# Performance work log

Hardware: AMD Instinct MI355X
Metric: run time of the kernel (lower is better)

The kernel has to match this reference:

```python
import jax, jax.numpy as jnp
import numpy as np

N0 = 16384; F_IN = 384; H = 512; E0 = 131072
DEPTH = 2; RATIO = 0.25; START_K = 6; K_INC = 1; INTERP_K = 6


def _pdist2(a, b):
    # squared euclidean distances [Na, Nb]
    d2 = jnp.sum(a * a, axis=1)[:, None] + jnp.sum(b * b, axis=1)[None, :] - 2.0 * (a @ b.T)
    return jnp.maximum(d2, 0.0)


def _fps(pos, n_keep):
    # farthest point sampling, deterministic start at node 0
    sel0 = jnp.zeros((n_keep,), jnp.int32)
    dist0 = jnp.sum((pos - pos[0]) ** 2, axis=-1)

    def body(i, st):
        sel, dist = st
        idx = jnp.argmax(dist).astype(jnp.int32)
        sel = sel.at[i].set(idx)
        dist = jnp.minimum(dist, jnp.sum((pos - pos[idx]) ** 2, axis=-1))
        return (sel, dist)

    sel, _ = jax.lax.fori_loop(1, n_keep, body, (sel0, dist0))
    return sel


def _knn_graph(pos, k):
    n = pos.shape[0]
    d2 = _pdist2(pos, pos)
    d2 = d2.at[jnp.arange(n), jnp.arange(n)].set(1e10)  # exclude self
    _, nbr = jax.lax.top_k(-d2, k)                      # [n, k] nearest neighbors
    src = nbr.reshape(-1)                               # flow: source_to_target
    dst = jnp.repeat(jnp.arange(n, dtype=nbr.dtype), k)
    return src, dst


def _gcn(x, src, dst, W, b):
    # GCNConv(improved=True): A_hat = D^-1/2 (A + 2I) D^-1/2, edge weights = 1
    n = x.shape[0]
    h = x @ W
    deg = jax.ops.segment_sum(jnp.ones(src.shape[0], x.dtype), dst, num_segments=n) + 2.0
    dinv = jax.lax.rsqrt(deg)
    coef = dinv[src] * dinv[dst]
    agg = jax.ops.segment_sum(h[src] * coef[:, None], dst, num_segments=n)
    agg = agg + h * (2.0 * dinv * dinv)[:, None]        # self loops with weight 2
    return agg + b


def _knn_interpolate(x, pos_x, pos_y, k):
    # interpolate coarse features x at pos_x onto fine positions pos_y (PyG knn_interpolate)
    d2 = _pdist2(pos_y, pos_x)                          # [Ny, Nx]
    negd, idx = jax.lax.top_k(-d2, k)                   # k nearest coarse points
    w = 1.0 / jnp.maximum(-negd, 1e-16)                 # [Ny, k]
    num = jnp.einsum('yk,ykf->yf', w, x[idx])
    return num / jnp.sum(w, axis=-1, keepdims=True)


def setup_inputs() -> dict:
    key = jax.random.key(0)
    ks = jax.random.split(key, 16)
    def w(k, fin, fout):
        return (jax.random.normal(k, (fin, fout), jnp.float32) / np.sqrt(fin)).astype(jnp.float32)
    return {
        'x': jax.random.normal(ks[0], (N0, F_IN), jnp.float32),
        'pos': jax.random.uniform(ks[1], (N0, 2), jnp.float32) * 100.0,
        'edge_index': jax.random.randint(ks[2], (2, E0), 0, N0, dtype=jnp.int32),
        'W_down0': w(ks[3], F_IN, H), 'b_down0': jnp.zeros((H,), jnp.float32),
        'W_down1': w(ks[4], H, H),   'b_down1': jnp.zeros((H,), jnp.float32),
        'W_up0': w(ks[5], H, H),     'b_up0': jnp.zeros((H,), jnp.float32),
        'W_up1': w(ks[6], H, H),     'b_up1': jnp.zeros((H,), jnp.float32),
        'W_lin': w(ks[7], H, H),     'b_lin': jnp.zeros((H,), jnp.float32),
    }


def reference(x, pos, edge_index, W_down0, b_down0, W_down1, b_down1,
              W_up0, b_up0, W_up1, b_up1, W_lin, b_lin):
    src, dst = edge_index[0], edge_index[1]
    Wd = [(W_down0, b_down0), (W_down1, b_down1)]
    Wu = [(W_up0, b_up0), (W_up1, b_up1)]
    all_pos = [pos]
    all_edges = [(src, dst)]
    for i in range(DEPTH):
        x = jax.nn.relu(_gcn(x, src, dst, *Wd[i]))
        n_keep = int(x.shape[0] * RATIO)
        perm = _fps(jax.lax.stop_gradient(pos), n_keep)
        pos = pos[perm]
        src, dst = _knn_graph(pos, START_K + i * K_INC)
        x = x[perm]
        all_pos.append(pos)
        all_edges.append((src, dst))
    for i in range(DEPTH):
        x = _knn_interpolate(x, all_pos[-i - 1], all_pos[-i - 2], INTERP_K)
        s, d = all_edges[-i - 2]
        x = jax.nn.relu(_gcn(x, s, d, *Wu[i]))
    return x @ W_lin + b_lin
```

## Files before the change

### kernel.cpp

```cpp
#include <hip/hip_runtime.h>

#define N0 16384
#define N1 4096
#define N2 1024
#define E0C 131072
#define FIN 384
#define HF 512

__device__ inline float4 f4fma(float w, const float4 v, float4 a) {
  a.x = fmaf(w, v.x, a.x); a.y = fmaf(w, v.y, a.y);
  a.z = fmaf(w, v.z, a.z); a.w = fmaf(w, v.w, a.w);
  return a;
}

__global__ __launch_bounds__(256)
void count_deg(const int* __restrict__ dst, int* __restrict__ cnt, int E) {
  int e = blockIdx.x * 256 + threadIdx.x;
  if (e < E) atomicAdd(&cnt[dst[e]], 1);
}

__global__ __launch_bounds__(1024)
void scan_offsets(const int* __restrict__ cnt, int* __restrict__ offs,
                  float* __restrict__ dinv) {
  __shared__ int ts[1024];
  const int t = threadIdx.x;
  int local[16];
  int sum = 0;
  #pragma unroll
  for (int j = 0; j < 16; ++j) { local[j] = cnt[t * 16 + j]; sum += local[j]; }
  ts[t] = sum;
  __syncthreads();
  for (int off = 1; off < 1024; off <<= 1) {
    int v = (t >= off) ? ts[t - off] : 0;
    __syncthreads();
    ts[t] += v;
    __syncthreads();
  }
  int run = ts[t] - sum;
  #pragma unroll
  for (int j = 0; j < 16; ++j) {
    offs[t * 16 + j] = run;
    dinv[t * 16 + j] = 1.0f / sqrtf((float)local[j] + 2.0f);
    run += local[j];
  }
  if (t == 1023) offs[N0] = run;
}

__global__ __launch_bounds__(256)
void fill_csr(const int* __restrict__ src, const int* __restrict__ dst,
              const int* __restrict__ offs, int* __restrict__ cursor,
              int* __restrict__ srcl, int E) {
  int e = blockIdx.x * 256 + threadIdx.x;
  if (e < E) {
    int d = dst[e];
    int p = atomicAdd(&cursor[d], 1);
    srcl[offs[d] + p] = src[e];
  }
}

template<int BM, int BN, int BK>
__global__ __launch_bounds__(256)
void gemm_f32(const float* __restrict__ A, const float* __restrict__ W,
              const float* __restrict__ bias, float* __restrict__ C,
              int M, int N, int K, int addBias) {
  __shared__ float As[BK][BM + 4];
  __shared__ float Ws[BK][BN];
  const int tid = threadIdx.x;
  const int bm = blockIdx.x * BM;
  const int bn = blockIdx.y * BN;
  const int tx = tid & 15;
  const int ty = tid >> 4;
  float acc[8][4];
  #pragma unroll
  for (int i = 0; i < 8; ++i)
    #pragma unroll
    for (int j = 0; j < 4; ++j) acc[i][j] = 0.f;

  for (int k0 = 0; k0 < K; k0 += BK) {
    #pragma unroll
    for (int h = 0; h < (BM * BK) / (256 * 4); ++h) {
      int q = tid + h * 256;
      int r = q >> 2;
      int c = (q & 3) << 2;
      float4 v = *(const float4*)(A + (size_t)(bm + r) * K + k0 + c);
      As[c][r] = v.x; As[c + 1][r] = v.y; As[c + 2][r] = v.z; As[c + 3][r] = v.w;
    }
    {
      int kk = tid >> 4;
      int n = (tid & 15) << 2;
      *(float4*)(&Ws[kk][n]) = *(const float4*)(W + (size_t)(k0 + kk) * N + bn + n);
    }
    __syncthreads();
    #pragma unroll
    for (int kk = 0; kk < BK; ++kk) {
      float4 b4 = *(const float4*)(&Ws[kk][tx << 2]);
      float4 a0 = *(const float4*)(&As[kk][ty << 3]);
      float4 a1 = *(const float4*)(&As[kk][(ty << 3) + 4]);
      float a[8] = {a0.x, a0.y, a0.z, a0.w, a1.x, a1.y, a1.z, a1.w};
      float b[4] = {b4.x, b4.y, b4.z, b4.w};
      #pragma unroll
      for (int i = 0; i < 8; ++i)
        #pragma unroll
        for (int j = 0; j < 4; ++j)
          acc[i][j] = fmaf(a[i], b[j], acc[i][j]);
    }
    __syncthreads();
  }
  #pragma unroll
  for (int i = 0; i < 8; ++i) {
    int row = bm + (ty << 3) + i;
    float4 o = {acc[i][0], acc[i][1], acc[i][2], acc[i][3]};
    if (addBias) {
      const float4 bb = *(const float4*)(bias + bn + (tx << 2));
      o.x += bb.x; o.y += bb.y; o.z += bb.z; o.w += bb.w;
    }
    *(float4*)(C + (size_t)row * N + bn + (tx << 2)) = o;
  }
}

__global__ __launch_bounds__(256)
void gcn_agg_csr(const float* __restrict__ h, const int* __restrict__ offs,
                 const int* __restrict__ srcl, const float* __restrict__ dinv,
                 const float* __restrict__ bias, float* __restrict__ out, int n) {
  const int wid = threadIdx.x >> 6, lane = threadIdx.x & 63;
  const int node = blockIdx.x * 4 + wid;
  if (node >= n) return;
  const float di = dinv[node];
  const int s0 = offs[node], s1 = offs[node + 1];
  float4 a0 = {0, 0, 0, 0}, a1 = {0, 0, 0, 0};
  for (int e = s0; e < s1; ++e) {
    const int s = srcl[e];
    const float w = dinv[s] * di;
    const float4* r = (const float4*)(h + (size_t)s * HF);
    a0 = f4fma(w, r[lane], a0);
    a1 = f4fma(w, r[64 + lane], a1);
  }
  const float sw = 2.0f * di * di;
  const float4* rs = (const float4*)(h + (size_t)node * HF);
  a0 = f4fma(sw, rs[lane], a0);
  a1 = f4fma(sw, rs[64 + lane], a1);
  const float4 b0 = *(const float4*)(bias + (lane << 2));
  const float4 b1 = *(const float4*)(bias + 256 + (lane << 2));
  a0.x = fmaxf(a0.x + b0.x, 0.f); a0.y = fmaxf(a0.y + b0.y, 0.f);
  a0.z = fmaxf(a0.z + b0.z, 0.f); a0.w = fmaxf(a0.w + b0.w, 0.f);
  a1.x = fmaxf(a1.x + b1.x, 0.f); a1.y = fmaxf(a1.y + b1.y, 0.f);
  a1.z = fmaxf(a1.z + b1.z, 0.f); a1.w = fmaxf(a1.w + b1.w, 0.f);
  float4* o = (float4*)(out + (size_t)node * HF);
  o[lane] = a0; o[64 + lane] = a1;
}

template<int K>
__global__ __launch_bounds__(256)
void gcn_agg_knn(const float* __restrict__ h, const int* __restrict__ nbr,
                 const float* __restrict__ bias, float* __restrict__ out, int n) {
  const int wid = threadIdx.x >> 6, lane = threadIdx.x & 63;
  const int node = blockIdx.x * 4 + wid;
  if (node >= n) return;
  const float di = 1.0f / sqrtf((float)(K + 2));
  const float w = di * di;
  float4 a0 = {0, 0, 0, 0}, a1 = {0, 0, 0, 0};
  #pragma unroll
  for (int j = 0; j < K; ++j) {
    const int s = nbr[node * K + j];
    const float4* r = (const float4*)(h + (size_t)s * HF);
    a0 = f4fma(w, r[lane], a0);
    a1 = f4fma(w, r[64 + lane], a1);
  }
  const float sw = 2.0f * di * di;
  const float4* rs = (const float4*)(h + (size_t)node * HF);
  a0 = f4fma(sw, rs[lane], a0);
  a1 = f4fma(sw, rs[64 + lane], a1);
  const float4 b0 = *(const float4*)(bias + (lane << 2));
  const float4 b1 = *(const float4*)(bias + 256 + (lane << 2));
  a0.x = fmaxf(a0.x + b0.x, 0.f); a0.y = fmaxf(a0.y + b0.y, 0.f);
  a0.z = fmaxf(a0.z + b0.z, 0.f); a0.w = fmaxf(a0.w + b0.w, 0.f);
  a1.x = fmaxf(a1.x + b1.x, 0.f); a1.y = fmaxf(a1.y + b1.y, 0.f);
  a1.z = fmaxf(a1.z + b1.z, 0.f); a1.w = fmaxf(a1.w + b1.w, 0.f);
  float4* o = (float4*)(out + (size_t)node * HF);
  o[lane] = a0; o[64 + lane] = a1;
}

__device__ __forceinline__ unsigned part1by1(unsigned x) {
  x &= 0xFFFFu;
  x = (x | (x << 8)) & 0x00FF00FFu;
  x = (x | (x << 4)) & 0x0F0F0F0Fu;
  x = (x | (x << 2)) & 0x33333333u;
  x = (x | (x << 1)) & 0x55555555u;
  return x;
}

__global__ __launch_bounds__(256)
void bin_hist(const float* __restrict__ pos, int* __restrict__ cid,
              int* __restrict__ hist, int n) {
  int i = blockIdx.x * 256 + threadIdx.x;
  if (i >= n) return;
  float x = pos[2 * i], y = pos[2 * i + 1];
  int cxi = (int)(x * 0.32f); cxi = cxi < 0 ? 0 : (cxi > 31 ? 31 : cxi);
  int cyi = (int)(y * 0.32f); cyi = cyi < 0 ? 0 : (cyi > 31 ? 31 : cyi);
  int c = (int)(part1by1((unsigned)cxi) | (part1by1((unsigned)cyi) << 1));
  cid[i] = c;
  atomicAdd(&hist[c], 1);
}

__global__ __launch_bounds__(1024)
void bin_scan(const int* __restrict__ hist, int* __restrict__ offs) {
  __shared__ int ts[1024];
  const int t = threadIdx.x;
  int v = hist[t];
  ts[t] = v;
  __syncthreads();
  for (int off = 1; off < 1024; off <<= 1) {
    int u = (t >= off) ? ts[t - off] : 0;
    __syncthreads();
    ts[t] += u;
    __syncthreads();
  }
  offs[t] = ts[t] - v;
  if (t == 1023) offs[1024] = ts[t];
}

__global__ __launch_bounds__(256)
void bin_scatter(const float* __restrict__ pos, const int* __restrict__ cid,
                 const int* __restrict__ offs, int* __restrict__ cursor,
                 float* __restrict__ sx, float* __restrict__ sy,
                 int* __restrict__ sid, int n) {
  int i = blockIdx.x * 256 + threadIdx.x;
  if (i >= n) return;
  int c = cid[i];
  int p = atomicAdd(&cursor[c], 1);
  int slot = offs[c] + p;
  sx[slot] = pos[2 * i];
  sy[slot] = pos[2 * i + 1];
  sid[slot] = i;
}

template<int NN>
__device__ __forceinline__ unsigned ror16(unsigned v) {
  return (unsigned)__builtin_amdgcn_update_dpp(0, (int)v, 0x120 | NN, 0xF, 0xF, false);
}

__device__ __forceinline__ void kcmp(unsigned& hi, unsigned& lo, float& x, float& y,
                                     unsigned ohi, unsigned olo, float ox, float oy) {
  unsigned long long a = ((unsigned long long)hi << 32) | lo;
  unsigned long long b = ((unsigned long long)ohi << 32) | olo;
  if (b > a) { hi = ohi; lo = olo; x = ox; y = oy; }
}

#define ROR_STEP(NN) { \
    unsigned ohi_ = ror16<NN>(hi), olo_ = ror16<NN>(lo); \
    unsigned ox_ = ror16<NN>(__float_as_uint(x)), oy_ = ror16<NN>(__float_as_uint(y)); \
    kcmp(hi, lo, x, y, ohi_, olo_, __uint_as_float(ox_), __uint_as_float(oy_)); }

__device__ __forceinline__ void wave_entry_reduce(
    unsigned long long ckey, float ccx, float ccy, int t, float4* wsc,
    unsigned& ehi, unsigned& elo, float& ex, float& ey) {
  unsigned hi = (unsigned)(ckey >> 32), lo = (unsigned)ckey;
  float x = ccx, y = ccy;
  ROR_STEP(1) ROR_STEP(2) ROR_STEP(4) ROR_STEP(8)
  if ((t & 15) == 0)
    wsc[(t >> 4) & 3] = make_float4(__uint_as_float(hi), __uint_as_float(lo), x, y);
  float4 a0 = wsc[0], a1 = wsc[1], a2 = wsc[2], a3 = wsc[3];
  hi = __float_as_uint(a0.x); lo = __float_as_uint(a0.y); x = a0.z; y = a0.w;
  kcmp(hi, lo, x, y, __float_as_uint(a1.x), __float_as_uint(a1.y), a1.z, a1.w);
  kcmp(hi, lo, x, y, __float_as_uint(a2.x), __float_as_uint(a2.y), a2.z, a2.w);
  kcmp(hi, lo, x, y, __float_as_uint(a3.x), __float_as_uint(a3.y), a3.z, a3.w);
  ehi = hi; elo = lo; ex = x; ey = y;
}

template<int N, int NT, int CPB, int SUBMAX, int NKEEP>
__global__ __launch_bounds__(NT, 1)
void fps_fast7(const float* __restrict__ pos0,
               const float* __restrict__ sx, const float* __restrict__ sy,
               const int* __restrict__ sid, const int* __restrict__ coffs,
               int* __restrict__ perm, float* __restrict__ pos_out) {
  constexpr int NW = NT / 64;
  const int t = threadIdx.x, wid = t >> 6, lane = t & 63;

  __shared__ float2 pp[N];
  __shared__ float4 ebuf[2][NW];
  __shared__ float4 wscr[NW][4];

  unsigned long long key[SUBMAX];

  const int start = coffs[wid * CPB];
  const int end   = coffs[wid * CPB + CPB];
  const int base  = start + lane;

  float cx = pos0[0], cy = pos0[1];
  if (t == 0) { perm[0] = 0; pos_out[0] = cx; pos_out[1] = cy; }

  float x0 = 3.4e38f, x1 = -3.4e38f, y0 = 3.4e38f, y1 = -3.4e38f;
  unsigned long long ckey = 0; float ccx = 0.f, ccy = 0.f;
  #pragma unroll
  for (int j = 0; j < SUBMAX; ++j) {
    int idx = base + j * 64;
    bool v = idx < end;
    int ridx = idx < (N - 1) ? idx : (N - 1);
    float qx = sx[ridx], qy = sy[ridx];
    unsigned uid = ~(unsigned)sid[ridx];
    if (v) {
      pp[idx] = make_float2(qx, qy);
      x0 = fminf(x0, qx); x1 = fmaxf(x1, qx);
      y0 = fminf(y0, qy); y1 = fmaxf(y1, qy);
    }
    float dx = __fsub_rn(qx, cx), dy = __fsub_rn(qy, cy);
    float nd = __fadd_rn(__fmul_rn(dx, dx), __fmul_rn(dy, dy));
    unsigned long long k =
        v ? (((unsigned long long)__float_as_uint(nd) << 32) | uid) : 0ull;
    key[j] = k;
    if (k > ckey) { ckey = k; ccx = qx; ccy = qy; }
  }

  #pragma unroll
  for (int m = 1; m < 64; m <<= 1) {
    x0 = fminf(x0, __shfl_xor(x0, m)); x1 = fmaxf(x1, __shfl_xor(x1, m));
    y0 = fminf(y0, __shfl_xor(y0, m)); y1 = fmaxf(y1, __shfl_xor(y1, m));
  }

  unsigned ehi, elo; float ex, ey;
  wave_entry_reduce(ckey, ccx, ccy, t, wscr[wid], ehi, elo, ex, ey);
  if (lane == 0)
    ebuf[0][wid] = make_float4(__uint_as_float(ehi), __uint_as_float(elo), ex, ey);
  __syncthreads();

  int p = 0;
  for (int i = 1; i < NKEEP; ++i) {
    float4 e = ebuf[p][t & (NW - 1)];
    unsigned hi = __float_as_uint(e.x), lo = __float_as_uint(e.y);
    float x = e.z, y = e.w;
    ROR_STEP(1)
    if constexpr (NW >= 4)  { ROR_STEP(2) }
    if constexpr (NW >= 8)  { ROR_STEP(4) }
    if constexpr (NW >= 16) { ROR_STEP(8) }
    if (t == 0) {
      perm[i] = (int)(~lo);
      pos_out[2 * i] = x; pos_out[2 * i + 1] = y;
    }
    cx = x; cy = y;

    float mdx = fmaxf(fmaxf(__fsub_rn(x0, cx), __fsub_rn(cx, x1)), 0.f);
    float mdy = fmaxf(fmaxf(__fsub_rn(y0, cy), __fsub_rn(cy, y1)), 0.f);
    float mb = mdx * mdx + mdy * mdy;
    if (!(mb * 0.99999f > __uint_as_float(ehi))) {
      unsigned long long bk = 0; float bx = 0.f, by = 0.f;
      #pragma unroll
      for (int j = 0; j < SUBMAX; ++j) {
        int idx = base + j * 64;
        int ridx = idx < (N - 1) ? idx : (N - 1);
        float2 q = pp[ridx];
        float dx = __fsub_rn(q.x, cx), dy = __fsub_rn(q.y, cy);
        float nd = __fadd_rn(__fmul_rn(dx, dx), __fmul_rn(dy, dy));
        unsigned long long nk =
            ((unsigned long long)__float_as_uint(nd) << 32) | (unsigned)key[j];
        if (nk < key[j]) key[j] = nk;
        if (key[j] > bk) { bk = key[j]; bx = q.x; by = q.y; }
      }
      wave_entry_reduce(bk, bx, by, t, wscr[wid], ehi, elo, ex, ey);
    }
    if (lane == 0)
      ebuf[p ^ 1][wid] = make_float4(__uint_as_float(ehi), __uint_as_float(elo), ex, ey);
    __syncthreads();
    p ^= 1;
  }
}

__global__ __launch_bounds__(256)
void gather_rows(const float* __restrict__ xin, const int* __restrict__ perm,
                 float* __restrict__ xout, int n) {
  const int wid = threadIdx.x >> 6, lane = threadIdx.x & 63;
  const int i = blockIdx.x * 4 + wid;
  if (i >= n) return;
  const int s = perm[i];
  const float4* r = (const float4*)(xin + (size_t)s * HF);
  float4* o = (float4*)(xout + (size_t)i * HF);
  o[lane] = r[lane];
  o[64 + lane] = r[64 + lane];
}

template<int NPTS, int K>
__global__ __launch_bounds__(256)
void knn_graph_kernel(const float* __restrict__ pos, int* __restrict__ srcout) {
  __shared__ float sx[NPTS], sy[NPTS], ss[NPTS];
  const int tid = threadIdx.x;
  for (int idx = tid; idx < NPTS; idx += 256) {
    float x = pos[2 * idx], y = pos[2 * idx + 1];
    sx[idx] = x; sy[idx] = y;
    ss[idx] = __fadd_rn(__fmul_rn(x, x), __fmul_rn(y, y));
  }
  __syncthreads();
  const int q = blockIdx.x * 256 + tid;
  const float qx = sx[q], qy = sy[q], qs = ss[q];
  float bd[K]; int bi[K];
  #pragma unroll
  for (int m = 0; m < K; ++m) { bd[m] = 3.4e38f; bi[m] = 0; }
  for (int j = 0; j < NPTS; ++j) {
    if (j == q) continue;
    float dot = __fadd_rn(__fmul_rn(qx, sx[j]), __fmul_rn(qy, sy[j]));
    float d2 = fmaxf(__fsub_rn(__fadd_rn(qs, ss[j]), __fmul_rn(2.0f, dot)), 0.0f);
    if (d2 < bd[K - 1]) {
      bool pr[K];
      #pragma unroll
      for (int m = 0; m < K; ++m) pr[m] = (d2 < bd[m]);
      #pragma unroll
      for (int m = K - 1; m >= 1; --m) {
        bd[m] = pr[m] ? (pr[m - 1] ? bd[m - 1] : d2) : bd[m];
        bi[m] = pr[m] ? (pr[m - 1] ? bi[m - 1] : j) : bi[m];
      }
      if (pr[0]) { bd[0] = d2; bi[0] = j; }
    }
  }
  #pragma unroll
  for (int m = 0; m < K; ++m) srcout[q * K + m] = bi[m];
}

template<int NX, int K>
__global__ __launch_bounds__(256)
void interp_topk(const float* __restrict__ posy, const float* __restrict__ posx,
                 int* __restrict__ oidx, float* __restrict__ ow,
                 float* __restrict__ owsum) {
  __shared__ float sx[NX], sy[NX], ss[NX];
  const int tid = threadIdx.x;
  for (int idx = tid; idx < NX; idx += 256) {
    float x = posx[2 * idx], y = posx[2 * idx + 1];
    sx[idx] = x; sy[idx] = y;
    ss[idx] = __fadd_rn(__fmul_rn(x, x), __fmul_rn(y, y));
  }
  __syncthreads();
  const int q = blockIdx.x * 256 + tid;
  const float qx = posy[2 * q], qy = posy[2 * q + 1];
  const float qs = __fadd_rn(__fmul_rn(qx, qx), __fmul_rn(qy, qy));
  float bd[K]; int bi[K];
  #pragma unroll
  for (int m = 0; m < K; ++m) { bd[m] = 3.4e38f; bi[m] = 0; }
  for (int j = 0; j < NX; ++j) {
    float dot = __fadd_rn(__fmul_rn(qx, sx[j]), __fmul_rn(qy, sy[j]));
    float d2 = fmaxf(__fsub_rn(__fadd_rn(qs, ss[j]), __fmul_rn(2.0f, dot)), 0.0f);
    if (d2 < bd[K - 1]) {
      bool pr[K];
      #pragma unroll
      for (int m = 0; m < K; ++m) pr[m] = (d2 < bd[m]);
      #pragma unroll
      for (int m = K - 1; m >= 1; --m) {
        bd[m] = pr[m] ? (pr[m - 1] ? bd[m - 1] : d2) : bd[m];
        bi[m] = pr[m] ? (pr[m - 1] ? bi[m - 1] : j) : bi[m];
      }
      if (pr[0]) { bd[0] = d2; bi[0] = j; }
    }
  }
  float wsum = 0.f;
  #pragma unroll
  for (int m = 0; m < K; ++m) {
    float w = 1.0f / fmaxf(bd[m], 1e-16f);
    ow[q * K + m] = w;
    oidx[q * K + m] = bi[m];
    wsum = __fadd_rn(wsum, w);
  }
  owsum[q] = wsum;
}

template<int K>
__global__ __launch_bounds__(256)
void interp_combine(const float* __restrict__ xin, const int* __restrict__ idx,
                    const float* __restrict__ w, const float* __restrict__ wsum,
                    float* __restrict__ out, int ny) {
  const int wid = threadIdx.x >> 6, lane = threadIdx.x & 63;
  const int q = blockIdx.x * 4 + wid;
  if (q >= ny) return;
  float4 a0 = {0, 0, 0, 0}, a1 = {0, 0, 0, 0};
  #pragma unroll
  for (int m = 0; m < K; ++m) {
    const int s = idx[q * K + m];
    const float wk = w[q * K + m];
    const float4* r = (const float4*)(xin + (size_t)s * HF);
    a0 = f4fma(wk, r[lane], a0);
    a1 = f4fma(wk, r[64 + lane], a1);
  }
  const float inv = wsum[q];
  a0.x /= inv; a0.y /= inv; a0.z /= inv; a0.w /= inv;
  a1.x /= inv; a1.y /= inv; a1.z /= inv; a1.w /= inv;
  float4* o = (float4*)(out + (size_t)q * HF);
  o[lane] = a0; o[64 + lane] = a1;
}

extern "C" void kernel_launch(void* const* d_in, const int* in_sizes, int n_in,
                              void* d_out, int out_size, void* d_ws, size_t ws_size,
                              hipStream_t stream) {
  const float* x    = (const float*)d_in[0];
  const float* pos  = (const float*)d_in[1];
  const int*   ei   = (const int*)d_in[2];
  const float* Wd0  = (const float*)d_in[3];
  const float* bd0  = (const float*)d_in[4];
  const float* Wd1  = (const float*)d_in[5];
  const float* bd1  = (const float*)d_in[6];
  const float* Wu0  = (const float*)d_in[7];
  const float* bu0  = (const float*)d_in[8];
  const float* Wu1  = (const float*)d_in[9];
  const float* bu1  = (const float*)d_in[10];
  const float* Wl   = (const float*)d_in[11];
  const float* bl   = (const float*)d_in[12];
  float* out = (float*)d_out;

  char* ws = (char*)d_ws;
  size_t off = 0;
  auto alloc = [&](size_t bytes) -> char* {
    char* p = ws + off;
    off = (off + bytes + 255) & ~(size_t)255;
    return p;
  };
  float* bufA   = (float*)alloc((size_t)N0 * HF * 4);
  float* bufB   = (float*)alloc((size_t)N0 * HF * 4);
  float* bufC   = (float*)alloc((size_t)N1 * HF * 4);
  float* x2     = (float*)alloc((size_t)N2 * HF * 4);
  int*   offs0  = (int*)alloc((N0 + 1) * 4);
  int*   srcl0  = (int*)alloc(E0C * 4);
  int*   cnt    = (int*)alloc(N0 * 4);
  int*   cursor = (int*)alloc(N0 * 4);
  float* dinv0  = (float*)alloc(N0 * 4);
  int*   perm0  = (int*)alloc(N1 * 4);
  float* pos1   = (float*)alloc(N1 * 2 * 4);
  int*   src1   = (int*)alloc(N1 * 6 * 4);
  int*   perm1  = (int*)alloc(N2 * 4);
  float* pos2   = (float*)alloc(N2 * 2 * 4);
  int*   iidx   = (int*)alloc((size_t)N0 * 6 * 4);
  float* iw     = (float*)alloc((size_t)N0 * 6 * 4);
  float* iwsum  = (float*)alloc(N0 * 4);
  float* bsx    = (float*)alloc(N0 * 4);
  float* bsy    = (float*)alloc(N0 * 4);
  int*   bsid   = (int*)alloc(N0 * 4);
  int*   bcid   = (int*)alloc(N0 * 4);
  int*   bhist  = (int*)alloc(1024 * 4);
  int*   bcur   = (int*)alloc(1024 * 4);
  int*   boffs  = (int*)alloc(1025 * 4);

  float* h1   = bufB;
  float* x1f  = bufB + (size_t)N1 * HF;
  float* hu0  = bufB;
  float* xu0f = bufB + (size_t)N1 * HF;

  hipMemsetAsync(cnt, 0, N0 * 4, stream);
  hipMemsetAsync(cursor, 0, N0 * 4, stream);
  count_deg<<<E0C / 256, 256, 0, stream>>>(ei + E0C, cnt, E0C);
  scan_offsets<<<1, 1024, 0, stream>>>(cnt, offs0, dinv0);
  fill_csr<<<E0C / 256, 256, 0, stream>>>(ei, ei + E0C, offs0, cursor, srcl0, E0C);

  hipMemsetAsync(bhist, 0, 1024 * 4, stream);
  hipMemsetAsync(bcur, 0, 1024 * 4, stream);
  bin_hist<<<N0 / 256, 256, 0, stream>>>(pos, bcid, bhist, N0);
  bin_scan<<<1, 1024, 0, stream>>>(bhist, boffs);
  bin_scatter<<<N0 / 256, 256, 0, stream>>>(pos, bcid, boffs, bcur, bsx, bsy, bsid, N0);

  gemm_f32<128, 64, 16><<<dim3(N0 / 128, HF / 64), 256, 0, stream>>>(
      x, Wd0, nullptr, bufA, N0, HF, FIN, 0);
  gcn_agg_csr<<<N0 / 4, 256, 0, stream>>>(bufA, offs0, srcl0, dinv0, bd0, bufB, N0);
  fps_fast7<N0, 1024, 64, 19, N1><<<1, 1024, 0, stream>>>(pos, bsx, bsy, bsid, boffs, perm0, pos1);
  gather_rows<<<N1 / 4, 256, 0, stream>>>(bufB, perm0, bufC, N1);
  knn_graph_kernel<N1, 6><<<N1 / 256, 256, 0, stream>>>(pos1, src1);

  hipMemsetAsync(bhist, 0, 1024 * 4, stream);
  hipMemsetAsync(bcur, 0, 1024 * 4, stream);
  bin_hist<<<N1 / 256, 256, 0, stream>>>(pos1, bcid, bhist, N1);
  bin_scan<<<1, 1024, 0, stream>>>(bhist, boffs);
  bin_scatter<<<N1 / 256, 256, 0, stream>>>(pos1, bcid, boffs, bcur, bsx, bsy, bsid, N1);

  gemm_f32<128, 64, 16><<<dim3(N1 / 128, HF / 64), 256, 0, stream>>>(
      bufC, Wd1, nullptr, h1, N1, HF, HF, 0);
  gcn_agg_knn<6><<<N1 / 4, 256, 0, stream>>>(h1, src1, bd1, x1f, N1);
  fps_fast7<N1, 512, 128, 10, N2><<<1, 512, 0, stream>>>(pos1, bsx, bsy, bsid, boffs, perm1, pos2);
  gather_rows<<<N2 / 4, 256, 0, stream>>>(x1f, perm1, x2, N2);

  interp_topk<N2, 6><<<N1 / 256, 256, 0, stream>>>(pos1, pos2, iidx, iw, iwsum);
  interp_combine<6><<<N1 / 4, 256, 0, stream>>>(x2, iidx, iw, iwsum, bufC, N1);
  gemm_f32<128, 64, 16><<<dim3(N1 / 128, HF / 64), 256, 0, stream>>>(
      bufC, Wu0, nullptr, hu0, N1, HF, HF, 0);
  gcn_agg_knn<6><<<N1 / 4, 256, 0, stream>>>(hu0, src1, bu0, xu0f, N1);

  interp_topk<N1, 6><<<N0 / 256, 256, 0, stream>>>(pos, pos1, iidx, iw, iwsum);
  interp_combine<6><<<N0 / 4, 256, 0, stream>>>(xu0f, iidx, iw, iwsum, bufA, N0);
  gemm_f32<128, 64, 16><<<dim3(N0 / 128, HF / 64), 256, 0, stream>>>(
      bufA, Wu1, nullptr, bufB, N0, HF, HF, 0);
  gcn_agg_csr<<<N0 / 4, 256, 0, stream>>>(bufB, offs0, srcl0, dinv0, bu1, bufA, N0);

  gemm_f32<128, 64, 16><<<dim3(N0 / 128, HF / 64), 256, 0, stream>>>(
      bufA, Wl, bl, out, N0, HF, HF, 1);
}
```

Baseline: 7.859 ms.

## Give each FPS wave several spatial sub-blocks with per-block bounding-box skipping

The farthest point sampling kernel now assigns multiple spatial cell groups (NSUB) to each wave. Each sub-block keeps its own bounding box and cached best key, so a wave skips the distance update per sub-block rather than for its whole region. Fewer waves (512 and 256 threads instead of 1024 and 512) shorten the per-iteration cross-wave reduction and barrier. The cost is more registers per thread and more serial work per wave when sub-blocks are not skipped.

```diff
diff --git a/kernel.cpp b/kernel.cpp
--- a/kernel.cpp
+++ b/kernel.cpp
@@ -267,9 +267,9 @@
   ehi = hi; elo = lo; ex = x; ey = y;
 }
 
-template<int N, int NT, int CPB, int SUBMAX, int NKEEP>
+template<int N, int NT, int NSUB, int CPB, int SUBMAX, int NKEEP>
 __global__ __launch_bounds__(NT, 1)
-void fps_fast7(const float* __restrict__ pos0,
+void fps_fast8(const float* __restrict__ pos0,
                const float* __restrict__ sx, const float* __restrict__ sy,
                const int* __restrict__ sid, const int* __restrict__ coffs,
                int* __restrict__ perm, float* __restrict__ pos_out) {
@@ -280,45 +280,54 @@
   __shared__ float4 ebuf[2][NW];
   __shared__ float4 wscr[NW][4];
 
-  unsigned long long key[SUBMAX];
-
-  const int start = coffs[wid * CPB];
-  const int end   = coffs[wid * CPB + CPB];
-  const int base  = start + lane;
+  unsigned long long key[NSUB * SUBMAX];
+  int   bstart[NSUB], bend[NSUB];
+  float bx0[NSUB], bx1[NSUB], by0[NSUB], by1[NSUB];
+  unsigned bthi[NSUB], btlo[NSUB]; float btx[NSUB], bty[NSUB];
 
   float cx = pos0[0], cy = pos0[1];
   if (t == 0) { perm[0] = 0; pos_out[0] = cx; pos_out[1] = cy; }
 
-  float x0 = 3.4e38f, x1 = -3.4e38f, y0 = 3.4e38f, y1 = -3.4e38f;
-  unsigned long long ckey = 0; float ccx = 0.f, ccy = 0.f;
-  #pragma unroll
-  for (int j = 0; j < SUBMAX; ++j) {
-    int idx = base + j * 64;
-    bool v = idx < end;
-    int ridx = idx < (N - 1) ? idx : (N - 1);
-    float qx = sx[ridx], qy = sy[ridx];
-    unsigned uid = ~(unsigned)sid[ridx];
-    if (v) {
-      pp[idx] = make_float2(qx, qy);
-      x0 = fminf(x0, qx); x1 = fmaxf(x1, qx);
-      y0 = fminf(y0, qy); y1 = fmaxf(y1, qy);
-    }
-    float dx = __fsub_rn(qx, cx), dy = __fsub_rn(qy, cy);
-    float nd = __fadd_rn(__fmul_rn(dx, dx), __fmul_rn(dy, dy));
-    unsigned long long k =
-        v ? (((unsigned long long)__float_as_uint(nd) << 32) | uid) : 0ull;
-    key[j] = k;
-    if (k > ckey) { ckey = k; ccx = qx; ccy = qy; }
-  }
-
-  #pragma unroll
-  for (int m = 1; m < 64; m <<= 1) {
-    x0 = fminf(x0, __shfl_xor(x0, m)); x1 = fmaxf(x1, __shfl_xor(x1, m));
-    y0 = fminf(y0, __shfl_xor(y0, m)); y1 = fmaxf(y1, __shfl_xor(y1, m));
-  }
-
-  unsigned ehi, elo; float ex, ey;
-  wave_entry_reduce(ckey, ccx, ccy, t, wscr[wid], ehi, elo, ex, ey);
+  #pragma unroll
+  for (int s = 0; s < NSUB; ++s) {
+    const int b = wid * NSUB + s;
+    const int start = coffs[b * CPB];
+    const int end   = coffs[b * CPB + CPB];
+    bstart[s] = start; bend[s] = end;
+    float x0 = 3.4e38f, x1 = -3.4e38f, y0 = 3.4e38f, y1 = -3.4e38f;
+    unsigned long long bk = 0; float bkx = 0.f, bky = 0.f;
+    #pragma unroll
+    for (int j = 0; j < SUBMAX; ++j) {
+      int idx = start + lane + j * 64;
+      bool v = idx < end;
+      int ridx = idx < (N - 1) ? idx : (N - 1);
+      float qx = sx[ridx], qy = sy[ridx];
+      unsigned uid = ~(unsigned)sid[ridx];
+      if (v) {
+        pp[idx] = make_float2(qx, qy);
+        x0 = fminf(x0, qx); x1 = fmaxf(x1, qx);
+        y0 = fminf(y0, qy); y1 = fmaxf(y1, qy);
+      }
+      float dx = __fsub_rn(qx, cx), dy = __fsub_rn(qy, cy);
+      float nd = __fadd_rn(__fmul_rn(dx, dx), __fmul_rn(dy, dy));
+      unsigned long long k =
+          v ? (((unsigned long long)__float_as_uint(nd) << 32) | uid) : 0ull;
+      key[s * SUBMAX + j] = k;
+      if (k > bk) { bk = k; bkx = qx; bky = qy; }
+    }
+    #pragma unroll
+    for (int m = 1; m < 64; m <<= 1) {
+      x0 = fminf(x0, __shfl_xor(x0, m)); x1 = fmaxf(x1, __shfl_xor(x1, m));
+      y0 = fminf(y0, __shfl_xor(y0, m)); y1 = fmaxf(y1, __shfl_xor(y1, m));
+    }
+    bx0[s] = x0; bx1[s] = x1; by0[s] = y0; by1[s] = y1;
+    wave_entry_reduce(bk, bkx, bky, t, wscr[wid], bthi[s], btlo[s], btx[s], bty[s]);
+  }
+
+  unsigned ehi = bthi[0], elo = btlo[0]; float ex = btx[0], ey = bty[0];
+  #pragma unroll
+  for (int s = 1; s < NSUB; ++s)
+    kcmp(ehi, elo, ex, ey, bthi[s], btlo[s], btx[s], bty[s]);
   if (lane == 0)
     ebuf[0][wid] = make_float4(__uint_as_float(ehi), __uint_as_float(elo), ex, ey);
   __syncthreads();
@@ -338,25 +347,34 @@
     }
     cx = x; cy = y;
 
-    float mdx = fmaxf(fmaxf(__fsub_rn(x0, cx), __fsub_rn(cx, x1)), 0.f);
-    float mdy = fmaxf(fmaxf(__fsub_rn(y0, cy), __fsub_rn(cy, y1)), 0.f);
-    float mb = mdx * mdx + mdy * mdy;
-    if (!(mb * 0.99999f > __uint_as_float(ehi))) {
-      unsigned long long bk = 0; float bx = 0.f, by = 0.f;
-      #pragma unroll
-      for (int j = 0; j < SUBMAX; ++j) {
-        int idx = base + j * 64;
-        int ridx = idx < (N - 1) ? idx : (N - 1);
-        float2 q = pp[ridx];
-        float dx = __fsub_rn(q.x, cx), dy = __fsub_rn(q.y, cy);
-        float nd = __fadd_rn(__fmul_rn(dx, dx), __fmul_rn(dy, dy));
-        unsigned long long nk =
-            ((unsigned long long)__float_as_uint(nd) << 32) | (unsigned)key[j];
-        if (nk < key[j]) key[j] = nk;
-        if (key[j] > bk) { bk = key[j]; bx = q.x; by = q.y; }
+    #pragma unroll
+    for (int s = 0; s < NSUB; ++s) {
+      float mdx = fmaxf(fmaxf(__fsub_rn(bx0[s], cx), __fsub_rn(cx, bx1[s])), 0.f);
+      float mdy = fmaxf(fmaxf(__fsub_rn(by0[s], cy), __fsub_rn(cy, by1[s])), 0.f);
+      float mb = mdx * mdx + mdy * mdy;
+      if (!(mb * 0.99999f > __uint_as_float(bthi[s]))) {
+        const int start = bstart[s];
+        unsigned long long bk = 0; float bkx = 0.f, bky = 0.f;
+        #pragma unroll
+        for (int j = 0; j < SUBMAX; ++j) {
+          int idx = start + lane + j * 64;
+          int ridx = idx < (N - 1) ? idx : (N - 1);
+          float2 q = pp[ridx];
+          float dx = __fsub_rn(q.x, cx), dy = __fsub_rn(q.y, cy);
+          float nd = __fadd_rn(__fmul_rn(dx, dx), __fmul_rn(dy, dy));
+          unsigned long long nk =
+              ((unsigned long long)__float_as_uint(nd) << 32) |
+              (unsigned)key[s * SUBMAX + j];
+          if (nk < key[s * SUBMAX + j]) key[s * SUBMAX + j] = nk;
+          if (key[s * SUBMAX + j] > bk) { bk = key[s * SUBMAX + j]; bkx = q.x; bky = q.y; }
+        }
+        wave_entry_reduce(bk, bkx, bky, t, wscr[wid], bthi[s], btlo[s], btx[s], bty[s]);
       }
-      wave_entry_reduce(bk, bx, by, t, wscr[wid], ehi, elo, ex, ey);
-    }
+    }
+    ehi = bthi[0]; elo = btlo[0]; ex = btx[0]; ey = bty[0];
+    #pragma unroll
+    for (int s = 1; s < NSUB; ++s)
+      kcmp(ehi, elo, ex, ey, bthi[s], btlo[s], btx[s], bty[s]);
     if (lane == 0)
       ebuf[p ^ 1][wid] = make_float4(__uint_as_float(ehi), __uint_as_float(elo), ex, ey);
     __syncthreads();
@@ -552,7 +570,8 @@
   gemm_f32<128, 64, 16><<<dim3(N0 / 128, HF / 64), 256, 0, stream>>>(
       x, Wd0, nullptr, bufA, N0, HF, FIN, 0);
   gcn_agg_csr<<<N0 / 4, 256, 0, stream>>>(bufA, offs0, srcl0, dinv0, bd0, bufB, N0);
-  fps_fast7<N0, 1024, 64, 19, N1><<<1, 1024, 0, stream>>>(pos, bsx, bsy, bsid, boffs, perm0, pos1);
+  fps_fast8<N0, 512, 2, 64, 19, N1><<<1, 512, 0, stream>>>(
+      pos, bsx, bsy, bsid, boffs, perm0, pos1);
   gather_rows<<<N1 / 4, 256, 0, stream>>>(bufB, perm0, bufC, N1);
   knn_graph_kernel<N1, 6><<<N1 / 256, 256, 0, stream>>>(pos1, src1);
 
@@ -565,7 +584,8 @@
   gemm_f32<128, 64, 16><<<dim3(N1 / 128, HF / 64), 256, 0, stream>>>(
       bufC, Wd1, nullptr, h1, N1, HF, HF, 0);
   gcn_agg_knn<6><<<N1 / 4, 256, 0, stream>>>(h1, src1, bd1, x1f, N1);
-  fps_fast7<N1, 512, 128, 10, N2><<<1, 512, 0, stream>>>(pos1, bsx, bsy, bsid, boffs, perm1, pos2);
+  fps_fast8<N1, 256, 4, 64, 7, N2><<<1, 256, 0, stream>>>(
+      pos1, bsx, bsy, bsid, boffs, perm1, pos2);
   gather_rows<<<N2 / 4, 256, 0, stream>>>(x1f, perm1, x2, N2);
 
   interp_topk<N2, 6><<<N1 / 256, 256, 0, stream>>>(pos1, pos2, iidx, iw, iwsum);
```

Result: slower. 8.167 ms (+3.9%).
